# Optimization experiments

Measured on AMD Instinct MI355X. Metric: run time of the kernel, lower is better.

Reference implementation:

```python
import jax, jax.numpy as jnp
import numpy as np

B, H, W, C = 16, 64, 64, 384
DH = 32                 # dim_head
NH = C // DH            # heads = dim // dim_head
WS = 8                  # window_size
DFF = 4 * C             # dim_ff default = 4*dim
EPS = 1e-5


def setup_inputs() -> dict:
    key = jax.random.key(0)
    ks = jax.random.split(key, 6)
    rn = lambda k, shape, scale: (jax.random.normal(k, shape, jnp.float32) * scale)
    return {
        "x": rn(ks[0], (B, H, W, C), 1.0),
        "w_qkv": rn(ks[1], (C, 3 * NH * DH), 0.02),   # fused qkv projection, bias=False
        "w_out": rn(ks[2], (NH * DH, C), 0.02),       # attention output projection
        "gamma_attn": jnp.ones((C,), jnp.float32),     # LayerNormNoBias2d weight (post-attn)
        "w1": rn(ks[3], (C, DFF), 0.02),               # FFN up projection
        "w2": rn(ks[4], (DFF, C), 0.02),               # FFN down projection
        "gamma_ff": jnp.ones((C,), jnp.float32),       # LayerNormNoBias2d weight (post-FFN)
    }


def _shift2d(x):
    # S2-MLP style 4-way spatial shift of channel quarters, zero-filled at borders.
    c4 = x.shape[-1] // 4
    g1 = jnp.pad(x[:, :-1, :, 0 * c4:1 * c4], ((0, 0), (1, 0), (0, 0), (0, 0)))  # shift down
    g2 = jnp.pad(x[:, 1:, :, 1 * c4:2 * c4], ((0, 0), (0, 1), (0, 0), (0, 0)))   # shift up
    g3 = jnp.pad(x[:, :, :-1, 2 * c4:3 * c4], ((0, 0), (0, 0), (1, 0), (0, 0)))  # shift right
    g4 = jnp.pad(x[:, :, 1:, 3 * c4:4 * c4], ((0, 0), (0, 0), (0, 1), (0, 0)))   # shift left
    return jnp.concatenate([g1, g2, g3, g4], axis=-1)


def _ln_nobias(x, gamma):
    # LayerNorm over channel dim, weight only (no bias).
    mu = jnp.mean(x, axis=-1, keepdims=True)
    var = jnp.var(x, axis=-1, keepdims=True)
    return (x - mu) * jax.lax.rsqrt(var + EPS) * gamma


def _window_attention(x, w_qkv, w_out):
    # Grouped (non-overlapping) window multi-head self-attention.
    b, h, w, c = x.shape
    nh, nw = h // WS, w // WS
    T = WS * WS
    # partition into windows: (b*nh*nw, T, c)
    xw = x.reshape(b, nh, WS, nw, WS, c).transpose(0, 1, 3, 2, 4, 5).reshape(b * nh * nw, T, c)
    qkv = xw @ w_qkv                                   # (n, T, 3*NH*DH)
    qkv = qkv.reshape(-1, T, 3, NH, DH)
    q = qkv[:, :, 0].transpose(0, 2, 1, 3)             # (n, NH, T, DH)
    k = qkv[:, :, 1].transpose(0, 2, 1, 3)
    v = qkv[:, :, 2].transpose(0, 2, 1, 3)
    logits = jnp.einsum('nhqd,nhkd->nhqk', q, k) * (DH ** -0.5)
    attn = jax.nn.softmax(logits, axis=-1)
    o = jnp.einsum('nhqk,nhkd->nhqd', attn, v)         # (n, NH, T, DH)
    o = o.transpose(0, 2, 1, 3).reshape(-1, T, NH * DH) @ w_out
    # un-window back to (b, h, w, c)
    return o.reshape(b, nh, nw, WS, WS, c).transpose(0, 1, 3, 2, 4, 5).reshape(b, h, w, c)


def reference(x, w_qkv, w_out, gamma_attn, w1, w2, gamma_ff):
    # x = x + DropBlock(Norm(GWAttn(Shift2d(x))))   (drop rates = 0 -> identity)
    a = _window_attention(_shift2d(x), w_qkv, w_out)
    x = x + _ln_nobias(a, gamma_attn)
    # x = x + DropBlock(Norm(FF(x)))
    f = jax.nn.gelu(x @ w1, approximate=False) @ w2
    return x + _ln_nobias(f, gamma_ff)
```

## Files before the change

### kernel.cpp

```cpp
#include <hip/hip_runtime.h>
#include <hip/hip_bf16.h>
#include <math.h>

typedef __attribute__((ext_vector_type(8))) __bf16 bf16x8;
typedef __attribute__((ext_vector_type(4))) float f32x4;
typedef unsigned int uint32;

static constexpr int kC   = 384;
static constexpr int kNH  = 12;
static constexpr int kDH  = 32;
static constexpr int kT   = 64;
static constexpr int kB   = 16;
static constexpr int kH   = 64;
static constexpr int kW   = 64;
static constexpr int kDFF = 1536;
static constexpr long kNTOK = 65536;
static constexpr long kNT  = kNTOK * kC;

__device__ __forceinline__ float bf_lo(uint32 u){ return __uint_as_float(u << 16); }
__device__ __forceinline__ float bf_hi(uint32 u){ return __uint_as_float(u & 0xffff0000u); }

__global__ void k_transpose_cast(const float* __restrict__ src, __bf16* __restrict__ dst,
                                 int K, int N)
{
    int o = blockIdx.x * 256 + threadIdx.x;
    if (o >= K * N) return;
    int n = o / K, k = o - n * K;
    dst[o] = (__bf16)src[(size_t)k * N + n];
}

__global__ __launch_bounds__(256) void k_shift_window(const float* __restrict__ x,
                                                      __bf16* __restrict__ Aw)
{
    int tid = blockIdx.x * 256 + threadIdx.x;
    int m = tid / 48;
    int g = tid - m * 48;
    int c0 = g * 8;
    int wi = m >> 6, t = m & 63;
    int b = wi >> 6, nh = (wi >> 3) & 7, nw = wi & 7;
    int h = nh * 8 + (t >> 3);
    int w = nw * 8 + (t & 7);
    int q = c0 / 96;
    int sh = h, sw = w;
    bool ok;
    if      (q == 0) { sh = h - 1; ok = (h >= 1);  }
    else if (q == 1) { sh = h + 1; ok = (h <= 62); }
    else if (q == 2) { sw = w - 1; ok = (w >= 1);  }
    else             { sw = w + 1; ok = (w <= 62); }

    __bf16 r[8] __attribute__((aligned(16)));
    if (ok) {
        const float4* src = reinterpret_cast<const float4*>(
            x + (((size_t)b * kH + sh) * kW + sw) * kC + c0);
        float4 v0 = src[0], v1 = src[1];
        r[0] = (__bf16)v0.x; r[1] = (__bf16)v0.y; r[2] = (__bf16)v0.z; r[3] = (__bf16)v0.w;
        r[4] = (__bf16)v1.x; r[5] = (__bf16)v1.y; r[6] = (__bf16)v1.z; r[7] = (__bf16)v1.w;
    } else {
        #pragma unroll
        for (int i = 0; i < 8; ++i) r[i] = (__bf16)0.0f;
    }
    *reinterpret_cast<int4*>(Aw + (size_t)m * kC + c0) = *reinterpret_cast<int4*>(r);
}

template<int EPI>
__global__ __launch_bounds__(256) void k_gemm(const __bf16* __restrict__ A,
                                              const __bf16* __restrict__ B,
                                              __bf16* __restrict__ Cout,
                                              int N, int K)
{
    __shared__ __bf16 As[128 * 32];
    __shared__ __bf16 Bs[128 * 32];
    const int tid  = threadIdx.x;
    const int wave = tid >> 6, lane = tid & 63;
    const int m0 = blockIdx.x * 128, n0 = blockIdx.y * 128;
    const int wr = (wave >> 1) * 64, wc = (wave & 1) * 64;

    f32x4 acc[4][4] = {};

    for (int k0 = 0; k0 < K; k0 += 32) {
        #pragma unroll
        for (int i = 0; i < 2; ++i) {
            int idx = tid + i * 256;
            int row = idx >> 2, seg = idx & 3;
            __builtin_amdgcn_global_load_lds(
                (const __attribute__((address_space(1))) void*)(A + (size_t)(m0 + row) * K + k0 + seg * 8),
                (__attribute__((address_space(3))) void*)(&As[idx * 8]), 16, 0, 0);
            __builtin_amdgcn_global_load_lds(
                (const __attribute__((address_space(1))) void*)(B + (size_t)(n0 + row) * K + k0 + seg * 8),
                (__attribute__((address_space(3))) void*)(&Bs[idx * 8]), 16, 0, 0);
        }
        asm volatile("s_waitcnt vmcnt(0)" ::: "memory");
        __syncthreads();

        bf16x8 af[4], bfr[4];
        #pragma unroll
        for (int mi = 0; mi < 4; ++mi)
            af[mi] = *reinterpret_cast<const bf16x8*>(&As[(wr + mi * 16 + (lane & 15)) * 32 + (lane >> 4) * 8]);
        #pragma unroll
        for (int ni = 0; ni < 4; ++ni)
            bfr[ni] = *reinterpret_cast<const bf16x8*>(&Bs[(wc + ni * 16 + (lane & 15)) * 32 + (lane >> 4) * 8]);
        #pragma unroll
        for (int mi = 0; mi < 4; ++mi)
            #pragma unroll
            for (int ni = 0; ni < 4; ++ni)
                acc[mi][ni] = __builtin_amdgcn_mfma_f32_16x16x32_bf16(af[mi], bfr[ni], acc[mi][ni], 0, 0, 0);
        __syncthreads();
    }

    #pragma unroll
    for (int mi = 0; mi < 4; ++mi) {
        #pragma unroll
        for (int ni = 0; ni < 4; ++ni) {
            #pragma unroll
            for (int r = 0; r < 4; ++r) {
                int row = m0 + wr + mi * 16 + ((lane >> 4) << 2) + r;
                int col = n0 + wc + ni * 16 + (lane & 15);
                float v = acc[mi][ni][r];
                if constexpr (EPI == 0) {
                    int s   = col / 384;
                    int rem = col - s * 384;
                    int hh  = rem >> 5, d = rem & 31;
                    Cout[(size_t)s * kNT + ((((size_t)(row >> 6)) * kNH + hh) * 64 + (row & 63)) * kDH + d] = (__bf16)v;
                } else if constexpr (EPI == 1) {
                    Cout[(size_t)row * N + col] = (__bf16)v;
                } else {
                    float gl = 0.5f * v * (1.0f + erff(v * 0.70710678118654752f));
                    Cout[(size_t)row * N + col] = (__bf16)gl;
                }
            }
        }
    }
}

__global__ __launch_bounds__(256) void k_attn(const __bf16* __restrict__ qkv,
                                              __bf16* __restrict__ AO)
{
    __shared__ __bf16 Pl[4][kT * kT];
    const int wave = threadIdx.x >> 6, lane = threadIdx.x & 63;
    const int pair = blockIdx.x * 4 + wave;
    const int wi = pair / kNH, hh = pair - wi * kNH;
    const int g = lane >> 4, qh = lane & 15;

    const __bf16* Qp = qkv + ((size_t)wi * kNH + hh) * (kT * kDH);
    const __bf16* Kp = Qp + kNT;
    const __bf16* Vp = Qp + 2 * kNT;
    char* Pb = (char*)&Pl[wave][0];

    bf16x8 qa[4], kb[4];
    #pragma unroll
    for (int mi = 0; mi < 4; ++mi)
        qa[mi] = *reinterpret_cast<const bf16x8*>(Qp + (mi * 16 + qh) * kDH + g * 8);
    #pragma unroll
    for (int ni = 0; ni < 4; ++ni)
        kb[ni] = *reinterpret_cast<const bf16x8*>(Kp + (ni * 16 + qh) * kDH + g * 8);

    f32x4 s[4][4] = {};
    #pragma unroll
    for (int mi = 0; mi < 4; ++mi)
        #pragma unroll
        for (int ni = 0; ni < 4; ++ni)
            s[mi][ni] = __builtin_amdgcn_mfma_f32_16x16x32_bf16(qa[mi], kb[ni], s[mi][ni], 0, 0, 0);

    const float scale = 0.17677669529663687f;
    float rmax[4][4], rsum[4][4];
    #pragma unroll
    for (int mi = 0; mi < 4; ++mi)
        #pragma unroll
        for (int r = 0; r < 4; ++r) {
            float a = fmaxf(fmaxf(s[mi][0][r], s[mi][1][r]), fmaxf(s[mi][2][r], s[mi][3][r]));
            #pragma unroll
            for (int st = 1; st < 16; st <<= 1) a = fmaxf(a, __shfl_xor(a, st));
            rmax[mi][r] = a;
        }
    #pragma unroll
    for (int mi = 0; mi < 4; ++mi)
        #pragma unroll
        for (int r = 0; r < 4; ++r) {
            float acc = 0.f;
            #pragma unroll
            for (int ni = 0; ni < 4; ++ni) {
                float p = __expf((s[mi][ni][r] - rmax[mi][r]) * scale);
                s[mi][ni][r] = p;
                acc += p;
            }
            #pragma unroll
            for (int st = 1; st < 16; st <<= 1) acc += __shfl_xor(acc, st);
            rsum[mi][r] = 1.0f / acc;
        }

    #pragma unroll
    for (int mi = 0; mi < 4; ++mi)
        #pragma unroll
        for (int ni = 0; ni < 4; ++ni)
            #pragma unroll
            for (int r = 0; r < 4; ++r) {
                int row = mi * 16 + g * 4 + r;
                int col = ni * 16 + qh;
                uint32 byte = (uint32)((row << 7) | (col << 1)) ^ (uint32)((row & 7) << 4);
                *reinterpret_cast<__bf16*>(Pb + byte) = (__bf16)s[mi][ni][r];
            }

    f32x4 o[4][2] = {};
    #pragma unroll
    for (int kk = 0; kk < 2; ++kk) {
        bf16x8 pa[4], vb[2];
        #pragma unroll
        for (int mi = 0; mi < 4; ++mi) {
            int row = mi * 16 + qh;
            uint32 byte = (uint32)((row << 7) | (kk << 6) | (g << 4)) ^ (uint32)((row & 7) << 4);
            pa[mi] = *reinterpret_cast<const bf16x8*>(Pb + byte);
        }
        #pragma unroll
        for (int n2 = 0; n2 < 2; ++n2) {
            __bf16 tmp[8];
            #pragma unroll
            for (int j = 0; j < 8; ++j)
                tmp[j] = Vp[(kk * 32 + g * 8 + j) * kDH + n2 * 16 + qh];
            vb[n2] = *reinterpret_cast<const bf16x8*>(tmp);
        }
        #pragma unroll
        for (int mi = 0; mi < 4; ++mi)
            #pragma unroll
            for (int n2 = 0; n2 < 2; ++n2)
                o[mi][n2] = __builtin_amdgcn_mfma_f32_16x16x32_bf16(pa[mi], vb[n2], o[mi][n2], 0, 0, 0);
    }

    #pragma unroll
    for (int mi = 0; mi < 4; ++mi)
        #pragma unroll
        for (int n2 = 0; n2 < 2; ++n2)
            #pragma unroll
            for (int r = 0; r < 4; ++r) {
                int row = mi * 16 + g * 4 + r;
                AO[((size_t)wi * 64 + row) * kC + hh * kDH + n2 * 16 + qh] =
                    (__bf16)(o[mi][n2][r] * rsum[mi][r]);
            }
}

__global__ __launch_bounds__(256) void k_ln_res1(const __bf16* __restrict__ P,
                                                 const float* __restrict__ x,
                                                 const float* __restrict__ gamma,
                                                 __bf16* __restrict__ X1)
{
    const int wave = threadIdx.x >> 6, lane = threadIdx.x & 63;
    const int tok = blockIdx.x * 4 + wave;
    const int b = tok >> 12, hw = tok & 4095, h = hw >> 6, w = hw & 63;
    const int m = (((b << 6) | ((h >> 3) << 3) | (w >> 3)) << 6) | (((h & 7) << 3) | (w & 7));

    float p[6]; float sum = 0.f, sq = 0.f;
    #pragma unroll
    for (int i = 0; i < 6; ++i) {
        p[i] = (float)P[(size_t)m * kC + lane + i * 64];
        sum += p[i]; sq += p[i] * p[i];
    }
    #pragma unroll
    for (int off = 32; off; off >>= 1) { sum += __shfl_xor(sum, off); sq += __shfl_xor(sq, off); }
    float mean = sum * (1.0f / kC);
    float var  = sq * (1.0f / kC) - mean * mean;
    float rs   = rsqrtf(var + 1e-5f);
    #pragma unroll
    for (int i = 0; i < 6; ++i) {
        int c = lane + i * 64;
        float v = x[(size_t)tok * kC + c] + (p[i] - mean) * rs * gamma[c];
        X1[(size_t)tok * kC + c] = (__bf16)v;
    }
}

__global__ __launch_bounds__(256) void k_ln_res2(const __bf16* __restrict__ F,
                                                 const __bf16* __restrict__ X1,
                                                 const float* __restrict__ gamma,
                                                 float* __restrict__ out)
{
    const int wave = threadIdx.x >> 6, lane = threadIdx.x & 63;
    const size_t tok = blockIdx.x * 4 + wave;

    float f[6]; float sum = 0.f, sq = 0.f;
    #pragma unroll
    for (int i = 0; i < 6; ++i) {
        f[i] = (float)F[tok * kC + lane + i * 64];
        sum += f[i]; sq += f[i] * f[i];
    }
    #pragma unroll
    for (int off = 32; off; off >>= 1) { sum += __shfl_xor(sum, off); sq += __shfl_xor(sq, off); }
    float mean = sum * (1.0f / kC);
    float var  = sq * (1.0f / kC) - mean * mean;
    float rs   = rsqrtf(var + 1e-5f);
    #pragma unroll
    for (int i = 0; i < 6; ++i) {
        int c = lane + i * 64;
        out[tok * kC + c] = (float)X1[tok * kC + c] + (f[i] - mean) * rs * gamma[c];
    }
}

extern "C" void kernel_launch(void* const* d_in, const int* in_sizes, int n_in,
                              void* d_out, int out_size, void* d_ws, size_t ws_size,
                              hipStream_t stream) {
    const float* x    = (const float*)d_in[0];
    const float* wqkv = (const float*)d_in[1];
    const float* wout = (const float*)d_in[2];
    const float* g_at = (const float*)d_in[3];
    const float* w1   = (const float*)d_in[4];
    const float* w2   = (const float*)d_in[5];
    const float* g_ff = (const float*)d_in[6];
    float* out = (float*)d_out;

    char* ws = (char*)d_ws;
    size_t off = 0;
    auto alloc = [&](size_t bytes) { size_t o = off; off += (bytes + 255) & ~(size_t)255; return o; };
    __bf16* WqkvT = (__bf16*)(ws + alloc((size_t)1152 * 384 * 2));
    __bf16* WoutT = (__bf16*)(ws + alloc((size_t)384 * 384 * 2));
    __bf16* W1T   = (__bf16*)(ws + alloc((size_t)1536 * 384 * 2));
    __bf16* W2T   = (__bf16*)(ws + alloc((size_t)384 * 1536 * 2));
    __bf16* R1    = (__bf16*)(ws + alloc((size_t)kNTOK * kDFF * 2));
    __bf16* R2    = (__bf16*)(ws + alloc((size_t)kNT * 2));
    __bf16* R3    = (__bf16*)(ws + alloc((size_t)kNT * 2));

    k_transpose_cast<<<dim3((384 * 1152 + 255) / 256), 256, 0, stream>>>(wqkv, WqkvT, 384, 1152);
    k_transpose_cast<<<dim3((384 * 384 + 255) / 256), 256, 0, stream>>>(wout, WoutT, 384, 384);
    k_transpose_cast<<<dim3((384 * 1536 + 255) / 256), 256, 0, stream>>>(w1, W1T, 384, 1536);
    k_transpose_cast<<<dim3((1536 * 384 + 255) / 256), 256, 0, stream>>>(w2, W2T, 1536, 384);

    k_shift_window<<<dim3(12288), 256, 0, stream>>>(x, R2);

    k_gemm<0><<<dim3(512, 9), 256, 0, stream>>>(R2, WqkvT, R1, 1152, 384);

    k_attn<<<dim3(3072), 256, 0, stream>>>(R1, R2);

    k_gemm<1><<<dim3(512, 3), 256, 0, stream>>>(R2, WoutT, R3, 384, 384);

    k_ln_res1<<<dim3(16384), 256, 0, stream>>>(R3, x, g_at, R2);

    k_gemm<2><<<dim3(512, 12), 256, 0, stream>>>(R2, W1T, R1, 1536, 384);

    k_gemm<1><<<dim3(512, 3), 256, 0, stream>>>(R1, W2T, R3, 384, 1536);

    k_ln_res2<<<dim3(16384), 256, 0, stream>>>(R3, R2, g_ff, out);
}
```

Measured before the change: 610.2 us.

## Double-buffer GEMM LDS tiles, swizzle LDS layout, remap blocks for XCD locality

The GEMM kernel now keeps two shared-memory buffers and issues the loads for the next K tile before computing on the current one, which drops one barrier per iteration and the explicit wait. LDS segments are XOR-swizzled to cut bank conflicts on the fragment reads. The grid becomes 1D, with a remap that spreads consecutive blocks across the 8 XCDs and orders N tiles fastest for cache reuse. The loop no longer has an explicit vmcnt wait before the barrier, so correctness depends on the compiler inserting the wait. It also doubles LDS use per block, which may reduce occupancy.

```diff
diff --git a/kernel.cpp b/kernel.cpp
--- a/kernel.cpp
+++ b/kernel.cpp
@@ -66,45 +66,62 @@
 __global__ __launch_bounds__(256) void k_gemm(const __bf16* __restrict__ A,
                                               const __bf16* __restrict__ B,
                                               __bf16* __restrict__ Cout,
-                                              int N, int K)
-{
-    __shared__ __bf16 As[128 * 32];
-    __shared__ __bf16 Bs[128 * 32];
+                                              int N, int K, int nt)
+{
+    __shared__ __align__(16) __bf16 As[2][128 * 32];
+    __shared__ __align__(16) __bf16 Bs[2][128 * 32];
     const int tid  = threadIdx.x;
     const int wave = tid >> 6, lane = tid & 63;
-    const int m0 = blockIdx.x * 128, n0 = blockIdx.y * 128;
+    const int g = lane >> 4, qh = lane & 15;
+
+    const int nwg = gridDim.x;
+    const int wg  = (blockIdx.x & 7) * (nwg >> 3) + (blockIdx.x >> 3);
+    const int nb  = wg % nt, mb = wg / nt;
+    const int m0 = mb * 128, n0 = nb * 128;
     const int wr = (wave >> 1) * 64, wc = (wave & 1) * 64;
 
-    f32x4 acc[4][4] = {};
-
-    for (int k0 = 0; k0 < K; k0 += 32) {
+    const int sw = ((g ^ ((lane >> 1) & 3)) << 3);
+
+    auto STAGE = [&](int buf, int k0) {
         #pragma unroll
         for (int i = 0; i < 2; ++i) {
             int idx = tid + i * 256;
-            int row = idx >> 2, seg = idx & 3;
+            int row = idx >> 2;
+            int gseg = (idx & 3) ^ ((idx >> 3) & 3);
             __builtin_amdgcn_global_load_lds(
-                (const __attribute__((address_space(1))) void*)(A + (size_t)(m0 + row) * K + k0 + seg * 8),
-                (__attribute__((address_space(3))) void*)(&As[idx * 8]), 16, 0, 0);
+                (const __attribute__((address_space(1))) void*)(A + (size_t)(m0 + row) * K + k0 + gseg * 8),
+                (__attribute__((address_space(3))) void*)(&As[buf][idx * 8]), 16, 0, 0);
             __builtin_amdgcn_global_load_lds(
-                (const __attribute__((address_space(1))) void*)(B + (size_t)(n0 + row) * K + k0 + seg * 8),
-                (__attribute__((address_space(3))) void*)(&Bs[idx * 8]), 16, 0, 0);
-        }
-        asm volatile("s_waitcnt vmcnt(0)" ::: "memory");
+                (const __attribute__((address_space(1))) void*)(B + (size_t)(n0 + row) * K + k0 + gseg * 8),
+                (__attribute__((address_space(3))) void*)(&Bs[buf][idx * 8]), 16, 0, 0);
+        }
+    };
+
+    f32x4 acc[4][4] = {};
+    const int nkt = K >> 5;
+
+    STAGE(0, 0);
+    for (int t = 0; t < nkt; ++t) {
+        const int cur = t & 1;
         __syncthreads();
+        if (t + 1 < nkt) STAGE(cur ^ 1, (t + 1) << 5);
 
         bf16x8 af[4], bfr[4];
         #pragma unroll
-        for (int mi = 0; mi < 4; ++mi)
-            af[mi] = *reinterpret_cast<const bf16x8*>(&As[(wr + mi * 16 + (lane & 15)) * 32 + (lane >> 4) * 8]);
-        #pragma unroll
-        for (int ni = 0; ni < 4; ++ni)
-            bfr[ni] = *reinterpret_cast<const bf16x8*>(&Bs[(wc + ni * 16 + (lane & 15)) * 32 + (lane >> 4) * 8]);
+        for (int mi = 0; mi < 4; ++mi) {
+            int ra = wr + mi * 16 + qh;
+            af[mi] = *reinterpret_cast<const bf16x8*>(&As[cur][ra * 32 + sw]);
+        }
+        #pragma unroll
+        for (int ni = 0; ni < 4; ++ni) {
+            int rb = wc + ni * 16 + qh;
+            bfr[ni] = *reinterpret_cast<const bf16x8*>(&Bs[cur][rb * 32 + sw]);
+        }
         #pragma unroll
         for (int mi = 0; mi < 4; ++mi)
             #pragma unroll
             for (int ni = 0; ni < 4; ++ni)
                 acc[mi][ni] = __builtin_amdgcn_mfma_f32_16x16x32_bf16(af[mi], bfr[ni], acc[mi][ni], 0, 0, 0);
-        __syncthreads();
     }
 
     #pragma unroll
@@ -113,8 +130,8 @@
         for (int ni = 0; ni < 4; ++ni) {
             #pragma unroll
             for (int r = 0; r < 4; ++r) {
-                int row = m0 + wr + mi * 16 + ((lane >> 4) << 2) + r;
-                int col = n0 + wc + ni * 16 + (lane & 15);
+                int row = m0 + wr + mi * 16 + (g << 2) + r;
+                int col = n0 + wc + ni * 16 + qh;
                 float v = acc[mi][ni][r];
                 if constexpr (EPI == 0) {
                     int s   = col / 384;
@@ -322,17 +339,17 @@
 
     k_shift_window<<<dim3(12288), 256, 0, stream>>>(x, R2);
 
-    k_gemm<0><<<dim3(512, 9), 256, 0, stream>>>(R2, WqkvT, R1, 1152, 384);
+    k_gemm<0><<<dim3(512 * 9), 256, 0, stream>>>(R2, WqkvT, R1, 1152, 384, 9);
 
     k_attn<<<dim3(3072), 256, 0, stream>>>(R1, R2);
 
-    k_gemm<1><<<dim3(512, 3), 256, 0, stream>>>(R2, WoutT, R3, 384, 384);
+    k_gemm<1><<<dim3(512 * 3), 256, 0, stream>>>(R2, WoutT, R3, 384, 384, 3);
 
     k_ln_res1<<<dim3(16384), 256, 0, stream>>>(R3, x, g_at, R2);
 
-    k_gemm<2><<<dim3(512, 12), 256, 0, stream>>>(R2, W1T, R1, 1536, 384);
-
-    k_gemm<1><<<dim3(512, 3), 256, 0, stream>>>(R1, W2T, R3, 384, 1536);
+    k_gemm<2><<<dim3(512 * 12), 256, 0, stream>>>(R2, W1T, R1, 1536, 384, 12);
+
+    k_gemm<1><<<dim3(512 * 3), 256, 0, stream>>>(R1, W2T, R3, 384, 1536, 3);
 
     k_ln_res2<<<dim3(16384), 256, 0, stream>>>(R3, R2, g_ff, out);
 }
```

Result: faster. 536.6 us (-12.1%).
